# Optimization experiments

Hardware: AMD Instinct MI355X
Metric: run time of the kernel (lower is better)

The kernel has to match this reference:

```python
import jax, jax.numpy as jnp
import numpy as np

B, C, N = 8, 2048, 512

def setup_inputs() -> dict:
    key = jax.random.key(0)
    ks = jax.random.split(key, 7)
    s = 1.0 / np.sqrt(N)
    return {
        "x":  jax.random.normal(ks[0], (B, C, N), dtype=jnp.float32),
        "Wq": jax.random.normal(ks[1], (N, N), dtype=jnp.float32) * s,
        "bq": jax.random.normal(ks[2], (N,), dtype=jnp.float32) * 0.01,
        "Wk": jax.random.normal(ks[3], (N, N), dtype=jnp.float32) * s,
        "bk": jax.random.normal(ks[4], (N,), dtype=jnp.float32) * 0.01,
        "Wv": jax.random.normal(ks[5], (N, N), dtype=jnp.float32) * s,
        "bv": jax.random.normal(ks[6], (N,), dtype=jnp.float32) * 0.01,
    }

def reference(x, Wq, bq, Wk, bk, Wv, bv):
    b, c, n = x.shape
    # QKV projections (torch Linear: x @ W.T + b)
    q = jnp.einsum('bcn,mn->bcm', x, Wq) + bq
    k = jnp.einsum('bcn,mn->bcm', x, Wk) + bk
    v = jnp.einsum('bcn,mn->bcm', x, Wv) + bv
    # attention over the C (token) dim: [b, c, c]
    attn = jnp.einsum('bcn,bdn->bcd', q, k)
    attn = jax.nn.softmax(attn, axis=-1) / jnp.sqrt(jnp.float32(n))
    # dropout is identity in eval mode
    out = jnp.einsum('bcd,bdn->bcn', attn, v)  # [b, c, n]
    # faithful to torch: .transpose(1, 2).reshape(B, C, N)
    score = jnp.transpose(out, (0, 2, 1)).reshape(b, c, n)
    return score
```

## Files before the change

kernel.cpp:

```cpp
#include <hip/hip_runtime.h>


typedef _Float16 half_t;
typedef __attribute__((ext_vector_type(8))) _Float16 half8;
typedef __attribute__((ext_vector_type(4))) _Float16 half4;
typedef __attribute__((ext_vector_type(4))) float    f32x4;

#define MFMA16x32(A_, B_, C_) __builtin_amdgcn_mfma_f32_16x16x32_f16((A_), (B_), (C_), 0, 0, 0)

__device__ __forceinline__ void gload_lds16(const void* g, void* l) {
  __builtin_amdgcn_global_load_lds(
      (const __attribute__((address_space(1))) void*)g,
      (__attribute__((address_space(3))) void*)l, 16, 0, 0);
}

__device__ __forceinline__ float dpp_max16(float x) {
  int t;
  t = __builtin_amdgcn_update_dpp(__float_as_int(x), __float_as_int(x), 0xB1, 0xF, 0xF, false);
  x = fmaxf(x, __int_as_float(t));
  t = __builtin_amdgcn_update_dpp(__float_as_int(x), __float_as_int(x), 0x4E, 0xF, 0xF, false);
  x = fmaxf(x, __int_as_float(t));
  t = __builtin_amdgcn_update_dpp(__float_as_int(x), __float_as_int(x), 0x124, 0xF, 0xF, false);
  x = fmaxf(x, __int_as_float(t));
  t = __builtin_amdgcn_update_dpp(__float_as_int(x), __float_as_int(x), 0x128, 0xF, 0xF, false);
  x = fmaxf(x, __int_as_float(t));
  return x;
}

__device__ __forceinline__ float dpp_sum16(float x) {
  int t;
  t = __builtin_amdgcn_update_dpp(__float_as_int(x), __float_as_int(x), 0xB1, 0xF, 0xF, false);
  x += __int_as_float(t);
  t = __builtin_amdgcn_update_dpp(__float_as_int(x), __float_as_int(x), 0x4E, 0xF, 0xF, false);
  x += __int_as_float(t);
  t = __builtin_amdgcn_update_dpp(__float_as_int(x), __float_as_int(x), 0x124, 0xF, 0xF, false);
  x += __int_as_float(t);
  t = __builtin_amdgcn_update_dpp(__float_as_int(x), __float_as_int(x), 0x128, 0xF, 0xF, false);
  x += __int_as_float(t);
  return x;
}

__global__ void cast_all(const float* __restrict__ x, const float* __restrict__ Wq,
                         const float* __restrict__ Wk, const float* __restrict__ Wv,
                         half_t* __restrict__ xh, half_t* __restrict__ wqh,
                         half_t* __restrict__ wkh, half_t* __restrict__ wvh) {
  int idx = blockIdx.x * 256 + threadIdx.x;
  const float* s;
  half_t* d;
  int off;
  if (idx < 2097152) { s = x; d = xh; off = idx; }
  else {
    int w = idx - 2097152;
    int which = w >> 16;
    off = w & 65535;
    s = (which == 0) ? Wq : (which == 1) ? Wk : Wv;
    d = (which == 0) ? wqh : (which == 1) ? wkh : wvh;
  }
  f32x4 v = ((const f32x4*)s)[off];
  half4 h;
#pragma unroll
  for (int j = 0; j < 4; ++j) h[j] = (_Float16)v[j];
  *(half4*)&d[(size_t)off * 4] = h;
}

template <int NKT, int SA, int SB, int MR>
__device__ __forceinline__ void gemm_core(
    const char* Abytes, const char* Bbytes,
    half_t* At, half_t* Bt, int tid, f32x4 (&acc)[MR][4]) {
  const int lane = tid & 63;
  const int wv = tid >> 6;
  const int g = lane >> 4, li = lane & 15;
  const int wm = wv >> 1, wn = wv & 1;
  const int ASTRIDE = MR * 2048;

  auto STAGE = [&](int kc, int buf) {
#pragma unroll
    for (int i2 = 0; i2 < MR; ++i2) {
      int seg = i2 * 256 + tid;
      int row = seg >> 3, blk = seg & 7;
      int bsrc = blk ^ (row & 7);
      gload_lds16(Abytes + ((size_t)row * SA + kc + bsrc * 8) * 2,
                  (void*)&At[buf * ASTRIDE + seg * 8]);
    }
#pragma unroll
    for (int i2 = 0; i2 < 4; ++i2) {
      int seg = i2 * 256 + tid;
      int row = seg >> 3, blk = seg & 7;
      int bsrc = blk ^ (row & 7);
      gload_lds16(Bbytes + ((size_t)row * SB + kc + bsrc * 8) * 2,
                  (void*)&Bt[buf * 8192 + seg * 8]);
    }
  };

  STAGE(0, 0);
  __syncthreads();
  int cur = 0;
#pragma unroll 1
  for (int kt = 0; kt < NKT; ++kt) {
    if (kt + 1 < NKT) STAGE((kt + 1) * 64, cur ^ 1);
#pragma unroll
    for (int kk = 0; kk < 2; ++kk) {
      half8 af[MR], bf[4];
#pragma unroll
      for (int i = 0; i < MR; ++i) {
        int ar = wm * (MR * 16) + i * 16 + li;
        af[i] = *(const half8*)&At[cur * ASTRIDE + ar * 64 + (((4 * kk + g) ^ (ar & 7)) * 8)];
      }
#pragma unroll
      for (int j = 0; j < 4; ++j) {
        int br = wn * 64 + j * 16 + li;
        bf[j] = *(const half8*)&Bt[cur * 8192 + br * 64 + (((4 * kk + g) ^ (br & 7)) * 8)];
      }
#pragma unroll
      for (int i = 0; i < MR; ++i)
#pragma unroll
        for (int j = 0; j < 4; ++j) acc[i][j] = MFMA16x32(af[i], bf[j], acc[i][j]);
    }
    __syncthreads();
    cur ^= 1;
  }
}

template <int MODE>
__global__ __launch_bounds__(256) void proj_gemm(
    const half_t* __restrict__ A, const half_t* __restrict__ Bm,
    const float* __restrict__ bias, half_t* __restrict__ out) {
  __shared__ half_t At[2 * 4 * 2048];
  __shared__ half_t Bt[2 * 8192];
  const int tid = threadIdx.x;
  const int lane = tid & 63, wv = tid >> 6;
  const int g = lane >> 4, li = lane & 15;
  const int wm = wv >> 1, wn = wv & 1;
  const int M0 = blockIdx.x * 128, N0 = blockIdx.y * 128;

  const f32x4 kZero = {0.f, 0.f, 0.f, 0.f};
  f32x4 acc[4][4];
#pragma unroll
  for (int i = 0; i < 4; ++i)
#pragma unroll
    for (int j = 0; j < 4; ++j) acc[i][j] = kZero;

  gemm_core<8, 512, 512, 4>((const char*)(A + (size_t)M0 * 512),
                            (const char*)(Bm + (size_t)N0 * 512), At, Bt, tid, acc);

  if (MODE == 2) {
#pragma unroll
    for (int i = 0; i < 4; ++i) {
      int trow = M0 + wm * 64 + i * 16 + 4 * g;
#pragma unroll
      for (int j = 0; j < 4; ++j) {
        int m = N0 + wn * 64 + j * 16 + li;
        float bs = bias[m];
#pragma unroll
        for (int r = 0; r < 4; ++r) {
          out[(size_t)(trow + r) * 512 + m] = (_Float16)(acc[i][j][r] + bs);
        }
      }
    }
  } else {
#pragma unroll
    for (int i = 0; i < 4; ++i) {
      int m0r = M0 + wm * 64 + i * 16 + 4 * g;
#pragma unroll
      for (int r = 0; r < 4; ++r) {
        int m = m0r + r;
        float bs = bias[m];
#pragma unroll
        for (int j = 0; j < 4; ++j) {
          int t = N0 + wn * 64 + j * 16 + li;
          out[(size_t)m * 16384 + t] = (_Float16)(acc[i][j][r] + bs);
        }
      }
    }
  }
}

__global__ __launch_bounds__(256) void s_softmax(
    const half_t* __restrict__ q, const half_t* __restrict__ k,
    half_t* __restrict__ Pp, float* __restrict__ m_t,
    float* __restrict__ m_fin, float* __restrict__ l_h) {
  __shared__ half_t At[64 * 512];
  __shared__ half_t Bt[2][64 * 64];
  const int tid = threadIdx.x;
  const int lane = tid & 63, wv = tid >> 6;
  const int g = lane >> 4, li = lane & 15;
  const int id = blockIdx.x;
  const int b = id & 7;
  const int rest = id >> 3;
  const int M0 = (rest >> 1) * 64;
  const int h = rest & 1;
  const int d0 = h * 1024;

  const char* qb = (const char*)(q + (size_t)(b * 2048 + M0) * 512);
  const char* kb = (const char*)(k + (size_t)(b * 2048 + d0) * 512);

#pragma unroll
  for (int i2 = 0; i2 < 16; ++i2) {
    int seg = i2 * 256 + tid;
    int row = seg >> 6, blk = seg & 63;
    int bsrc = blk ^ (row & 7);
    gload_lds16(qb + ((size_t)row * 512 + bsrc * 8) * 2, (void*)&At[seg * 8]);
  }

  auto BSTAGE = [&](int it, int buf) {
    int dt = it >> 3, ks = it & 7;
#pragma unroll
    for (int i2 = 0; i2 < 2; ++i2) {
      int seg = i2 * 256 + tid;
      int row = seg >> 3, blk = seg & 7;
      int bsrc = blk ^ (row & 7);
      gload_lds16(kb + ((size_t)(dt * 64 + row) * 512 + ks * 64 + bsrc * 8) * 2,
                  (void*)&Bt[buf][seg * 8]);
    }
  };
  BSTAGE(0, 0);
  __syncthreads();

  const int ar = wv * 16 + li;
  const int swzA = ar & 7;
  const f32x4 kZero = {0.f, 0.f, 0.f, 0.f};
  float m_run[4] = {-3e38f, -3e38f, -3e38f, -3e38f};
  float l_run[4] = {0.f, 0.f, 0.f, 0.f};
  f32x4 acc[4];
  int cur = 0;

#pragma unroll 1
  for (int it = 0; it < 128; ++it) {
    const int dt = it >> 3, ks = it & 7;
    if (ks == 0) {
#pragma unroll
      for (int j = 0; j < 4; ++j) acc[j] = kZero;
    }
    if (it + 1 < 128) BSTAGE(it + 1, cur ^ 1);

#pragma unroll
    for (int kk = 0; kk < 2; ++kk) {
      half8 af = *(const half8*)&At[ar * 512 + (((ks * 8 + kk * 4 + g) ^ swzA) * 8)];
#pragma unroll
      for (int j = 0; j < 4; ++j) {
        int br = j * 16 + li;
        half8 bf = *(const half8*)&Bt[cur][br * 64 + (((kk * 4 + g) ^ (br & 7)) * 8)];
        acc[j] = MFMA16x32(af, bf, acc[j]);
      }
    }

    if (ks == 7) {
      float mnew[4], alpha[4], tsum[4];
#pragma unroll
      for (int r = 0; r < 4; ++r) {
        float tm = fmaxf(fmaxf(acc[0][r], acc[1][r]), fmaxf(acc[2][r], acc[3][r]));
        tm = dpp_max16(tm);
        mnew[r] = fmaxf(m_run[r], tm);
        alpha[r] = __expf(m_run[r] - mnew[r]);
        tsum[r] = 0.f;
      }
      const size_t prow0 = (size_t)(b * 2048 + M0 + wv * 16);
#pragma unroll
      for (int j = 0; j < 4; ++j) {
#pragma unroll
        for (int r = 0; r < 4; ++r) {
          float p = __expf(acc[j][r] - mnew[r]);
          tsum[r] += p;
          Pp[(prow0 + 4 * g + r) * 2048 + d0 + dt * 64 + j * 16 + li] = (_Float16)p;
        }
      }
#pragma unroll
      for (int r = 0; r < 4; ++r) {
        float ts = dpp_sum16(tsum[r]);
        l_run[r] = l_run[r] * alpha[r] + ts;
        m_run[r] = mnew[r];
      }
      if (li == 0) {
#pragma unroll
        for (int r = 0; r < 4; ++r)
          m_t[(prow0 + 4 * g + r) * 32 + h * 16 + dt] = mnew[r];
      }
    }

    __syncthreads();
    cur ^= 1;
  }

  if (li == 0) {
    const size_t prow0 = (size_t)(b * 2048 + M0 + wv * 16);
#pragma unroll
    for (int r = 0; r < 4; ++r) {
      m_fin[(prow0 + 4 * g + r) * 2 + h] = m_run[r];
      l_h[(prow0 + 4 * g + r) * 2 + h] = l_run[r];
    }
  }
}

__global__ void sm_merge(const float* __restrict__ m_fin, const float* __restrict__ l_h,
                         float* __restrict__ m_glob, float* __restrict__ l_fin) {
  int rr = blockIdx.x * 256 + threadIdx.x;
  float m0 = m_fin[rr * 2], m1 = m_fin[rr * 2 + 1];
  float mg = fmaxf(m0, m1);
  l_fin[rr] = l_h[rr * 2] * __expf(m0 - mg) + l_h[rr * 2 + 1] * __expf(m1 - mg);
  m_glob[rr] = mg;
}

__global__ __launch_bounds__(256) void pv_gemm(
    const half_t* __restrict__ Pp, const half_t* __restrict__ vt,
    const float* __restrict__ m_t, const float* __restrict__ m_glob,
    const float* __restrict__ l_fin, float* __restrict__ outp) {
  __shared__ half_t At[2][2 * 2048];
  __shared__ half_t Bt[2][8192];
  __shared__ float  sc[64][33];
  const int tid = threadIdx.x;
  const int lane = tid & 63, wv = tid >> 6;
  const int g = lane >> 4, li = lane & 15;
  const int wm = wv >> 1, wn = wv & 1;
  const int id = blockIdx.x;
  const int b = id & 7;
  const int idx = id >> 3;
  const int M0 = (idx >> 2) * 64;
  const int N0 = (idx & 3) * 128;
  const int rgb = b * 2048 + M0;

#pragma unroll
  for (int i2 = 0; i2 < 8; ++i2) {
    int e = i2 * 256 + tid;
    int row = e >> 5, kt = e & 31;
    sc[row][kt] = __expf(m_t[(size_t)(rgb + row) * 32 + kt] - m_glob[rgb + row]);
  }

  const half_t* Pb = Pp + (size_t)rgb * 2048;
  const char* Bb = (const char*)(vt + (size_t)N0 * 16384 + (size_t)b * 2048);

  auto BSTAGE = [&](int kt, int buf) {
#pragma unroll
    for (int i2 = 0; i2 < 4; ++i2) {
      int seg = i2 * 256 + tid;
      int row = seg >> 3, blk = seg & 7;
      int bsrc = blk ^ (row & 7);
      gload_lds16(Bb + ((size_t)row * 16384 + kt * 64 + bsrc * 8) * 2,
                  (void*)&Bt[buf][seg * 8]);
    }
  };
  const int s0row = tid >> 3, s0blk = tid & 7;
  const int s1row = (256 + tid) >> 3, s1blk = tid & 7;

  __syncthreads();

  half8 a0 = *(const half8*)&Pb[(size_t)s0row * 2048 + s0blk * 8];
  half8 a1 = *(const half8*)&Pb[(size_t)s1row * 2048 + s1blk * 8];
  BSTAGE(0, 0);
  {
    _Float16 f0 = (_Float16)sc[s0row][0], f1 = (_Float16)sc[s1row][0];
#pragma unroll
    for (int e = 0; e < 8; ++e) { a0[e] *= f0; a1[e] *= f1; }
    *(half8*)&At[0][s0row * 64 + ((s0blk ^ (s0row & 7)) * 8)] = a0;
    *(half8*)&At[0][s1row * 64 + ((s1blk ^ (s1row & 7)) * 8)] = a1;
  }
  __syncthreads();

  const f32x4 kZero = {0.f, 0.f, 0.f, 0.f};
  f32x4 acc[2][4];
#pragma unroll
  for (int i = 0; i < 2; ++i)
#pragma unroll
    for (int j = 0; j < 4; ++j) acc[i][j] = kZero;

  int cur = 0;
#pragma unroll 1
  for (int kt = 0; kt < 32; ++kt) {
    half8 n0, n1;
    if (kt + 1 < 32) {
      n0 = *(const half8*)&Pb[(size_t)s0row * 2048 + (kt + 1) * 64 + s0blk * 8];
      n1 = *(const half8*)&Pb[(size_t)s1row * 2048 + (kt + 1) * 64 + s1blk * 8];
      BSTAGE(kt + 1, cur ^ 1);
    }
#pragma unroll
    for (int kk = 0; kk < 2; ++kk) {
      half8 af[2], bf[4];
#pragma unroll
      for (int i = 0; i < 2; ++i) {
        int arr = wm * 32 + i * 16 + li;
        af[i] = *(const half8*)&At[cur][arr * 64 + (((4 * kk + g) ^ (arr & 7)) * 8)];
      }
#pragma unroll
      for (int j = 0; j < 4; ++j) {
        int br = wn * 64 + j * 16 + li;
        bf[j] = *(const half8*)&Bt[cur][br * 64 + (((4 * kk + g) ^ (br & 7)) * 8)];
      }
#pragma unroll
      for (int i = 0; i < 2; ++i)
#pragma unroll
        for (int j = 0; j < 4; ++j) acc[i][j] = MFMA16x32(af[i], bf[j], acc[i][j]);
    }
    if (kt + 1 < 32) {
      _Float16 f0 = (_Float16)sc[s0row][kt + 1], f1 = (_Float16)sc[s1row][kt + 1];
#pragma unroll
      for (int e = 0; e < 8; ++e) { n0[e] *= f0; n1[e] *= f1; }
      *(half8*)&At[cur ^ 1][s0row * 64 + ((s0blk ^ (s0row & 7)) * 8)] = n0;
      *(half8*)&At[cur ^ 1][s1row * 64 + ((s1blk ^ (s1row & 7)) * 8)] = n1;
    }
    __syncthreads();
    cur ^= 1;
  }

#pragma unroll
  for (int i = 0; i < 2; ++i) {
    int c0r = M0 + wm * 32 + i * 16 + 4 * g;
    float inv[4];
#pragma unroll
    for (int r = 0; r < 4; ++r)
      inv[r] = 1.0f / (l_fin[b * 2048 + c0r + r] * 22.62741699796952f);
#pragma unroll
    for (int j = 0; j < 4; ++j) {
      int n = N0 + wn * 64 + j * 16 + li;
      float* ob = outp + (size_t)b * 1048576 + (size_t)n * 2048 + c0r;
#pragma unroll
      for (int r = 0; r < 4; ++r) {
        ob[r] = acc[i][j][r] * inv[r];
      }
    }
  }
}

extern "C" void kernel_launch(void* const* d_in, const int* in_sizes, int n_in,
                              void* d_out, int out_size, void* d_ws, size_t ws_size,
                              hipStream_t stream) {
  const float* x  = (const float*)d_in[0];
  const float* Wq = (const float*)d_in[1];
  const float* bq = (const float*)d_in[2];
  const float* Wk = (const float*)d_in[3];
  const float* bk = (const float*)d_in[4];
  const float* Wv = (const float*)d_in[5];
  const float* bv = (const float*)d_in[6];

  half_t* qsb  = (half_t*)d_ws;
  half_t* ksb  = qsb + (size_t)16384 * 512;
  half_t* vtb  = ksb + (size_t)16384 * 512;
  half_t* Pp   = vtb + (size_t)512 * 16384;
  half_t* xh   = Pp;
  half_t* wqh  = xh  + (size_t)16384 * 512;
  half_t* wkh  = wqh + (size_t)512 * 512;
  half_t* wvh  = wkh + (size_t)512 * 512;
  float*  m_t  = (float*)(Pp + (size_t)16384 * 2048);
  float*  m_fin = m_t + (size_t)16384 * 32;
  float*  l_hb  = m_fin + (size_t)16384 * 2;
  float*  m_glb = l_hb + (size_t)16384 * 2;
  float*  l_fin = m_glb + (size_t)16384;

  cast_all<<<dim3(8960), 256, 0, stream>>>(x, Wq, Wk, Wv, xh, wqh, wkh, wvh);

  proj_gemm<2><<<dim3(128, 4), 256, 0, stream>>>(xh, wqh, bq, qsb);
  proj_gemm<2><<<dim3(128, 4), 256, 0, stream>>>(xh, wkh, bk, ksb);
  proj_gemm<1><<<dim3(4, 128), 256, 0, stream>>>(wvh, xh, bv, vtb);

  s_softmax<<<dim3(512), 256, 0, stream>>>(qsb, ksb, Pp, m_t, m_fin, l_hb);
  sm_merge<<<dim3(64), 256, 0, stream>>>(m_fin, l_hb, m_glb, l_fin);
  pv_gemm<<<dim3(1024), 256, 0, stream>>>(Pp, vtb, m_t, m_glb, l_fin,
                                          (float*)d_out);
}
```

Before: 216.6 us.

## Split QK^T softmax into independent 64x128 tiles with per-tile max and sum

Replaces the streaming online-softmax kernel, which ran 512 blocks each sweeping 1024 key columns sequentially, with 4096 independent blocks. Each block computes a 64x128 score tile through the shared gemm_core, takes the tile-local row max and sum, and writes exp values plus per-tile statistics. The merge kernel now combines 16 tile maxima per row and precomputes the rescale factors, and pv_gemm reads those factors directly, using one per pair of 64-wide k-steps. This is meant to raise parallelism and occupancy and to remove the long serialized loop. In exchange it adds more m_t/l_t traffic and recomputes nothing, but it relies on gemm_core's tiling matching a 128-column tile.

```diff
diff --git a/kernel.cpp b/kernel.cpp
--- a/kernel.cpp
+++ b/kernel.cpp
@@ -26,7 +26,6 @@
   x = fmaxf(x, __int_as_float(t));
   return x;
 }
-
 __device__ __forceinline__ float dpp_sum16(float x) {
   int t;
   t = __builtin_amdgcn_update_dpp(__float_as_int(x), __float_as_int(x), 0xB1, 0xF, 0xF, false);
@@ -175,138 +174,117 @@
   }
 }
 
-__global__ __launch_bounds__(256) void s_softmax(
+__global__ __launch_bounds__(256) void s_pmax(
     const half_t* __restrict__ q, const half_t* __restrict__ k,
-    half_t* __restrict__ Pp, float* __restrict__ m_t,
-    float* __restrict__ m_fin, float* __restrict__ l_h) {
-  __shared__ half_t At[64 * 512];
-  __shared__ half_t Bt[2][64 * 64];
+    half_t* __restrict__ Pp, float* __restrict__ m_t, float* __restrict__ l_t) {
+  __shared__ half_t At[2 * 2 * 2048];
+  __shared__ half_t Bt[2 * 8192];
+  __shared__ float  mx2[2][64];
+  __shared__ float  sm2[2][64];
   const int tid = threadIdx.x;
   const int lane = tid & 63, wv = tid >> 6;
   const int g = lane >> 4, li = lane & 15;
+  const int wm = wv >> 1, wn = wv & 1;
   const int id = blockIdx.x;
   const int b = id & 7;
-  const int rest = id >> 3;
-  const int M0 = (rest >> 1) * 64;
-  const int h = rest & 1;
-  const int d0 = h * 1024;
-
-  const char* qb = (const char*)(q + (size_t)(b * 2048 + M0) * 512);
-  const char* kb = (const char*)(k + (size_t)(b * 2048 + d0) * 512);
-
-#pragma unroll
-  for (int i2 = 0; i2 < 16; ++i2) {
-    int seg = i2 * 256 + tid;
-    int row = seg >> 6, blk = seg & 63;
-    int bsrc = blk ^ (row & 7);
-    gload_lds16(qb + ((size_t)row * 512 + bsrc * 8) * 2, (void*)&At[seg * 8]);
-  }
-
-  auto BSTAGE = [&](int it, int buf) {
-    int dt = it >> 3, ks = it & 7;
-#pragma unroll
-    for (int i2 = 0; i2 < 2; ++i2) {
-      int seg = i2 * 256 + tid;
-      int row = seg >> 3, blk = seg & 7;
-      int bsrc = blk ^ (row & 7);
-      gload_lds16(kb + ((size_t)(dt * 64 + row) * 512 + ks * 64 + bsrc * 8) * 2,
-                  (void*)&Bt[buf][seg * 8]);
-    }
-  };
-  BSTAGE(0, 0);
+  const int idx = id >> 3;
+  const int M0 = (idx & 31) * 64;
+  const int N0 = (idx >> 5) * 128;
+  const int tile = idx >> 5;
+
+  const f32x4 kZero = {0.f, 0.f, 0.f, 0.f};
+  f32x4 acc[2][4];
+#pragma unroll
+  for (int i = 0; i < 2; ++i)
+#pragma unroll
+    for (int j = 0; j < 4; ++j) acc[i][j] = kZero;
+
+  gemm_core<8, 512, 512, 2>(
+      (const char*)(q + (size_t)(b * 2048 + M0) * 512),
+      (const char*)(k + (size_t)(b * 2048 + N0) * 512), At, Bt, tid, acc);
+
+  float lmax[2][4];
+#pragma unroll
+  for (int i = 0; i < 2; ++i)
+#pragma unroll
+    for (int r = 0; r < 4; ++r) {
+      float v = fmaxf(fmaxf(acc[0 + i][0][r], acc[i][1][r]),
+                      fmaxf(acc[i][2][r], acc[i][3][r]));
+      lmax[i][r] = dpp_max16(v);
+    }
+  if (li == 0) {
+#pragma unroll
+    for (int i = 0; i < 2; ++i)
+#pragma unroll
+      for (int r = 0; r < 4; ++r)
+        mx2[wn][wm * 32 + i * 16 + 4 * g + r] = lmax[i][r];
+  }
   __syncthreads();
 
-  const int ar = wv * 16 + li;
-  const int swzA = ar & 7;
-  const f32x4 kZero = {0.f, 0.f, 0.f, 0.f};
-  float m_run[4] = {-3e38f, -3e38f, -3e38f, -3e38f};
-  float l_run[4] = {0.f, 0.f, 0.f, 0.f};
-  f32x4 acc[4];
-  int cur = 0;
-
-#pragma unroll 1
-  for (int it = 0; it < 128; ++it) {
-    const int dt = it >> 3, ks = it & 7;
-    if (ks == 0) {
-#pragma unroll
-      for (int j = 0; j < 4; ++j) acc[j] = kZero;
-    }
-    if (it + 1 < 128) BSTAGE(it + 1, cur ^ 1);
-
-#pragma unroll
-    for (int kk = 0; kk < 2; ++kk) {
-      half8 af = *(const half8*)&At[ar * 512 + (((ks * 8 + kk * 4 + g) ^ swzA) * 8)];
+  const size_t grow0 = (size_t)(b * 2048 + M0 + wm * 32);
+  float tsum[2][4];
+#pragma unroll
+  for (int i = 0; i < 2; ++i) {
+#pragma unroll
+    for (int r = 0; r < 4; ++r) {
+      int lr = wm * 32 + i * 16 + 4 * g + r;
+      float m = fmaxf(mx2[0][lr], mx2[1][lr]);
+      float s = 0.f;
 #pragma unroll
       for (int j = 0; j < 4; ++j) {
-        int br = j * 16 + li;
-        half8 bf = *(const half8*)&Bt[cur][br * 64 + (((kk * 4 + g) ^ (br & 7)) * 8)];
-        acc[j] = MFMA16x32(af, bf, acc[j]);
-      }
-    }
-
-    if (ks == 7) {
-      float mnew[4], alpha[4], tsum[4];
+        float p = __expf(acc[i][j][r] - m);
+        s += p;
+        Pp[(grow0 + i * 16 + 4 * g + r) * 2048 + N0 + wn * 64 + j * 16 + li] =
+            (_Float16)p;
+      }
+      tsum[i][r] = dpp_sum16(s);
+      lmax[i][r] = m;
+    }
+  }
+  if (li == 0) {
+#pragma unroll
+    for (int i = 0; i < 2; ++i)
+#pragma unroll
+      for (int r = 0; r < 4; ++r)
+        sm2[wn][wm * 32 + i * 16 + 4 * g + r] = tsum[i][r];
+  }
+  __syncthreads();
+  if (wn == 0 && li == 0) {
+#pragma unroll
+    for (int i = 0; i < 2; ++i)
 #pragma unroll
       for (int r = 0; r < 4; ++r) {
-        float tm = fmaxf(fmaxf(acc[0][r], acc[1][r]), fmaxf(acc[2][r], acc[3][r]));
-        tm = dpp_max16(tm);
-        mnew[r] = fmaxf(m_run[r], tm);
-        alpha[r] = __expf(m_run[r] - mnew[r]);
-        tsum[r] = 0.f;
-      }
-      const size_t prow0 = (size_t)(b * 2048 + M0 + wv * 16);
-#pragma unroll
-      for (int j = 0; j < 4; ++j) {
-#pragma unroll
-        for (int r = 0; r < 4; ++r) {
-          float p = __expf(acc[j][r] - mnew[r]);
-          tsum[r] += p;
-          Pp[(prow0 + 4 * g + r) * 2048 + d0 + dt * 64 + j * 16 + li] = (_Float16)p;
-        }
-      }
-#pragma unroll
-      for (int r = 0; r < 4; ++r) {
-        float ts = dpp_sum16(tsum[r]);
-        l_run[r] = l_run[r] * alpha[r] + ts;
-        m_run[r] = mnew[r];
-      }
-      if (li == 0) {
-#pragma unroll
-        for (int r = 0; r < 4; ++r)
-          m_t[(prow0 + 4 * g + r) * 32 + h * 16 + dt] = mnew[r];
-      }
-    }
-
-    __syncthreads();
-    cur ^= 1;
-  }
-
-  if (li == 0) {
-    const size_t prow0 = (size_t)(b * 2048 + M0 + wv * 16);
-#pragma unroll
-    for (int r = 0; r < 4; ++r) {
-      m_fin[(prow0 + 4 * g + r) * 2 + h] = m_run[r];
-      l_h[(prow0 + 4 * g + r) * 2 + h] = l_run[r];
-    }
-  }
-}
-
-__global__ void sm_merge(const float* __restrict__ m_fin, const float* __restrict__ l_h,
-                         float* __restrict__ m_glob, float* __restrict__ l_fin) {
+        int lr = wm * 32 + i * 16 + 4 * g + r;
+        m_t[(grow0 + i * 16 + 4 * g + r) * 16 + tile] = lmax[i][r];
+        l_t[(grow0 + i * 16 + 4 * g + r) * 16 + tile] = sm2[0][lr] + sm2[1][lr];
+      }
+  }
+}
+
+__global__ void sm_merge(const float* __restrict__ m_t, const float* __restrict__ l_t,
+                         float* __restrict__ sc_g, float* __restrict__ l_fin) {
   int rr = blockIdx.x * 256 + threadIdx.x;
-  float m0 = m_fin[rr * 2], m1 = m_fin[rr * 2 + 1];
-  float mg = fmaxf(m0, m1);
-  l_fin[rr] = l_h[rr * 2] * __expf(m0 - mg) + l_h[rr * 2 + 1] * __expf(m1 - mg);
-  m_glob[rr] = mg;
+  float m[16];
+  float mg = -3e38f;
+#pragma unroll
+  for (int t = 0; t < 16; ++t) { m[t] = m_t[rr * 16 + t]; mg = fmaxf(mg, m[t]); }
+  float l = 0.f;
+#pragma unroll
+  for (int t = 0; t < 16; ++t) {
+    float s = __expf(m[t] - mg);
+    sc_g[rr * 16 + t] = s;
+    l += l_t[rr * 16 + t] * s;
+  }
+  l_fin[rr] = l;
 }
 
 __global__ __launch_bounds__(256) void pv_gemm(
     const half_t* __restrict__ Pp, const half_t* __restrict__ vt,
-    const float* __restrict__ m_t, const float* __restrict__ m_glob,
-    const float* __restrict__ l_fin, float* __restrict__ outp) {
+    const float* __restrict__ sc_g, const float* __restrict__ l_fin,
+    float* __restrict__ outp) {
   __shared__ half_t At[2][2 * 2048];
   __shared__ half_t Bt[2][8192];
-  __shared__ float  sc[64][33];
+  __shared__ float  sc[64][17];
   const int tid = threadIdx.x;
   const int lane = tid & 63, wv = tid >> 6;
   const int g = lane >> 4, li = lane & 15;
@@ -319,10 +297,10 @@
   const int rgb = b * 2048 + M0;
 
 #pragma unroll
-  for (int i2 = 0; i2 < 8; ++i2) {
+  for (int i2 = 0; i2 < 4; ++i2) {
     int e = i2 * 256 + tid;
-    int row = e >> 5, kt = e & 31;
-    sc[row][kt] = __expf(m_t[(size_t)(rgb + row) * 32 + kt] - m_glob[rgb + row]);
+    int row = e >> 4, t = e & 15;
+    sc[row][t] = sc_g[(size_t)(rgb + row) * 16 + t];
   }
 
   const half_t* Pb = Pp + (size_t)rgb * 2048;
@@ -390,7 +368,8 @@
         for (int j = 0; j < 4; ++j) acc[i][j] = MFMA16x32(af[i], bf[j], acc[i][j]);
     }
     if (kt + 1 < 32) {
-      _Float16 f0 = (_Float16)sc[s0row][kt + 1], f1 = (_Float16)sc[s1row][kt + 1];
+      _Float16 f0 = (_Float16)sc[s0row][(kt + 1) >> 1];
+      _Float16 f1 = (_Float16)sc[s1row][(kt + 1) >> 1];
 #pragma unroll
       for (int e = 0; e < 8; ++e) { n0[e] *= f0; n1[e] *= f1; }
       *(half8*)&At[cur ^ 1][s0row * 64 + ((s0blk ^ (s0row & 7)) * 8)] = n0;
@@ -439,10 +418,9 @@
   half_t* wkh  = wqh + (size_t)512 * 512;
   half_t* wvh  = wkh + (size_t)512 * 512;
   float*  m_t  = (float*)(Pp + (size_t)16384 * 2048);
-  float*  m_fin = m_t + (size_t)16384 * 32;
-  float*  l_hb  = m_fin + (size_t)16384 * 2;
-  float*  m_glb = l_hb + (size_t)16384 * 2;
-  float*  l_fin = m_glb + (size_t)16384;
+  float*  l_t  = m_t + (size_t)16384 * 16;
+  float*  sc_g = l_t + (size_t)16384 * 16;
+  float*  l_fin = sc_g + (size_t)16384 * 16;
 
   cast_all<<<dim3(8960), 256, 0, stream>>>(x, Wq, Wk, Wv, xh, wqh, wkh, wvh);
 
@@ -450,8 +428,7 @@
   proj_gemm<2><<<dim3(128, 4), 256, 0, stream>>>(xh, wkh, bk, ksb);
   proj_gemm<1><<<dim3(4, 128), 256, 0, stream>>>(wvh, xh, bv, vtb);
 
-  s_softmax<<<dim3(512), 256, 0, stream>>>(qsb, ksb, Pp, m_t, m_fin, l_hb);
-  sm_merge<<<dim3(64), 256, 0, stream>>>(m_fin, l_hb, m_glb, l_fin);
-  pv_gemm<<<dim3(1024), 256, 0, stream>>>(Pp, vtb, m_t, m_glb, l_fin,
-                                          (float*)d_out);
-}
+  s_pmax<<<dim3(4096), 256, 0, stream>>>(qsb, ksb, Pp, m_t, l_t);
+  sm_merge<<<dim3(64), 256, 0, stream>>>(m_t, l_t, sc_g, l_fin);
+  pv_gemm<<<dim3(1024), 256, 0, stream>>>(Pp, vtb, sc_g, l_fin, (float*)d_out);
+}
```

Result: faster. 177.7 us (-17.9%).
